# Kernel tuning notes

Measured on AMD Instinct MI355X. Metric: run time of the kernel, lower is better.

The kernel has to match this reference:

```python
import jax, jax.numpy as jnp
import numpy as np

B, S, D, F, E = 2, 1024, 1024, 4096, 8

def setup_inputs() -> dict:
    key = jax.random.key(0)
    ks = jax.random.split(key, 6)
    sc = 0.02  # typical init scale
    return {
        "sequences": jax.random.normal(ks[0], (B, S, D), jnp.float32),
        "router_w1": jax.random.normal(ks[1], (D, D), jnp.float32) * sc,
        "router_b1": jnp.zeros((D,), jnp.float32),
        "router_w2": jax.random.normal(ks[2], (D, E), jnp.float32) * sc,
        "router_b2": jnp.zeros((E,), jnp.float32),
        "expert_w1": jax.random.normal(ks[3], (E, D, F), jnp.float32) * sc,
        "expert_b1": jnp.zeros((E, F), jnp.float32),
        "expert_w2": jax.random.normal(ks[4], (E, F, D), jnp.float32) * sc,
        "expert_b2": jnp.zeros((E, D), jnp.float32),
    }

def reference(sequences, router_w1, router_b1, router_w2, router_b2,
              expert_w1, expert_b1, expert_w2, expert_b2):
    # Router: Linear -> ReLU -> Linear -> Softmax, per-token argmax expert pick
    h = jax.nn.relu(sequences @ router_w1 + router_b1)          # [B,S,D]
    probs = jax.nn.softmax(h @ router_w2 + router_b2, axis=-1)  # [B,S,E]
    idx = jnp.argmax(probs, axis=-1)                            # [B,S] int
    onehot = jax.nn.one_hot(idx, expert_w1.shape[0], dtype=sequences.dtype)  # [B,S,E]
    # Dense all-expert FFN (2-layer position-wise FC w/ ReLU, dropout=0 eval),
    # then combine with the one-hot selection (hard top-1 dispatch semantics).
    hid = jax.nn.relu(jnp.einsum('bsd,edf->ebsf', sequences, expert_w1)
                      + expert_b1[:, None, None, :])            # [E,B,S,F]
    y = jnp.einsum('ebsf,efd->ebsd', hid, expert_w2) + expert_b2[:, None, None, :]
    return jnp.einsum('ebsd,bse->bsd', y, onehot)               # [B,S,D]
```

## Files before the change

kernel.cpp:

```cpp
#include <hip/hip_runtime.h>
#include <hip/hip_bf16.h>

#define T_TOK 2048
#define DD 1024
#define FF 4096
#define EE 8

typedef __attribute__((ext_vector_type(8))) short short8;
typedef __attribute__((ext_vector_type(4))) short short4v;
typedef __attribute__((ext_vector_type(4))) float floatx4;

static __device__ __forceinline__ unsigned f2bf_u(float f){
  unsigned u = __float_as_uint(f);
  unsigned r = u + 0x7fffu + ((u >> 16) & 1u);
  return r >> 16;
}

static __device__ __forceinline__ short8 ldfrag(const unsigned short* p){
  short4v lo = *(const short4v*)p;
  short4v hi = *(const short4v*)(p + 4);
  return __builtin_shufflevector(lo, hi, 0, 1, 2, 3, 4, 5, 6, 7);
}

__global__ __launch_bounds__(256) void router_gemm1(
    const float* __restrict__ X, const float* __restrict__ W,
    const float* __restrict__ bias, float* __restrict__ H, int* counts)
{
  if (blockIdx.x == 0 && blockIdx.y == 0 && threadIdx.x < EE) counts[threadIdx.x] = 0;
  __shared__ float As[2][16][68];
  __shared__ float Bs[2][16][68];
  const int tid = threadIdx.x;
  const int tx = tid & 15, ty = tid >> 4;
  const int bm = blockIdx.y * 64, bn = blockIdx.x * 64;
  const int ar = tid >> 2, ak = (tid & 3) * 4;
  const int bk = tid >> 4, bn0 = (tid & 15) * 4;
  const float* aP = X + (size_t)(bm + ar) * DD;
  float acc[4][4] = {};
  float4 pa, pb;

  pa = *(const float4*)(aP + ak);
  pb = *(const float4*)(W + (size_t)bk * DD + bn + bn0);
  As[0][ak+0][ar] = pa.x; As[0][ak+1][ar] = pa.y;
  As[0][ak+2][ar] = pa.z; As[0][ak+3][ar] = pa.w;
  *(float4*)&Bs[0][bk][bn0] = pb;
  __syncthreads();

  for (int it = 0; it < DD/16; ++it){
    if (it + 1 < DD/16){
      const int kt = (it + 1) * 16;
      pa = *(const float4*)(aP + kt + ak);
      pb = *(const float4*)(W + (size_t)(kt + bk) * DD + bn + bn0);
    }
    const int buf = it & 1;
    #pragma unroll
    for (int k = 0; k < 16; ++k){
      float4 av = *(const float4*)&As[buf][k][ty*4];
      float4 bv = *(const float4*)&Bs[buf][k][tx*4];
      float am[4] = {av.x, av.y, av.z, av.w};
      float bm4[4] = {bv.x, bv.y, bv.z, bv.w};
      #pragma unroll
      for (int i = 0; i < 4; ++i)
        #pragma unroll
        for (int j = 0; j < 4; ++j)
          acc[i][j] += am[i] * bm4[j];
    }
    if (it + 1 < DD/16){
      const int nb2 = (it + 1) & 1;
      As[nb2][ak+0][ar] = pa.x; As[nb2][ak+1][ar] = pa.y;
      As[nb2][ak+2][ar] = pa.z; As[nb2][ak+3][ar] = pa.w;
      *(float4*)&Bs[nb2][bk][bn0] = pb;
      __syncthreads();
    }
  }
  #pragma unroll
  for (int i = 0; i < 4; ++i){
    float4 v;
    v.x = fmaxf(acc[i][0] + bias[bn + tx*4 + 0], 0.f);
    v.y = fmaxf(acc[i][1] + bias[bn + tx*4 + 1], 0.f);
    v.z = fmaxf(acc[i][2] + bias[bn + tx*4 + 2], 0.f);
    v.w = fmaxf(acc[i][3] + bias[bn + tx*4 + 3], 0.f);
    *(float4*)(H + (size_t)(bm + ty*4 + i) * DD + bn + tx*4) = v;
  }
}

__global__ __launch_bounds__(64) void router_logits_argmax(
    const float* __restrict__ H, const float* __restrict__ W2,
    const float* __restrict__ b2, int* __restrict__ eidx, int* __restrict__ counts)
{
  const int t = blockIdx.x;
  const int lane = threadIdx.x;
  const float* h = H + (size_t)t * DD;
  float acc[8] = {0,0,0,0,0,0,0,0};
  for (int d = lane; d < DD; d += 64){
    float hv = h[d];
    float4 w0 = *(const float4*)(W2 + (size_t)d * 8);
    float4 w1 = *(const float4*)(W2 + (size_t)d * 8 + 4);
    acc[0] += hv * w0.x; acc[1] += hv * w0.y; acc[2] += hv * w0.z; acc[3] += hv * w0.w;
    acc[4] += hv * w1.x; acc[5] += hv * w1.y; acc[6] += hv * w1.z; acc[7] += hv * w1.w;
  }
  #pragma unroll
  for (int s = 32; s > 0; s >>= 1)
    #pragma unroll
    for (int e2 = 0; e2 < 8; ++e2)
      acc[e2] += __shfl_down(acc[e2], s, 64);
  if (lane == 0){
    int best = 0; float bv = acc[0] + b2[0];
    #pragma unroll
    for (int e2 = 1; e2 < 8; ++e2){
      float v = acc[e2] + b2[e2];
      if (v > bv){ bv = v; best = e2; }
    }
    eidx[t] = best;
    atomicAdd(&counts[best], 1);
  }
}

__global__ void scan_offsets(const int* __restrict__ counts, int* __restrict__ offsets,
                             int* __restrict__ cursors)
{
  if (threadIdx.x == 0 && blockIdx.x == 0){
    int s = 0;
    for (int e = 0; e < EE; ++e){ offsets[e] = s; cursors[e] = s; s += counts[e]; }
    offsets[EE] = s;
  }
}

__global__ __launch_bounds__(256) void scatter_tokens(
    const int* __restrict__ eidx, int* __restrict__ cursors, int* __restrict__ perm)
{
  int t = blockIdx.x * 256 + threadIdx.x;
  if (t < T_TOK){
    int e = eidx[t];
    int p = atomicAdd(&cursors[e], 1);
    perm[p] = t;
  }
}

template<bool FIRST>
__global__ __launch_bounds__(256) void expert_gemm(
    const float* __restrict__ X,
    const unsigned short* __restrict__ hidIn,
    const float* __restrict__ Wall,
    const float* __restrict__ Ball,
    unsigned short* __restrict__ hidOut,
    float* __restrict__ Yout,
    const int* __restrict__ perm,
    const int* __restrict__ offsets)
{
  constexpr int K = FIRST ? DD : FF;
  constexpr int N = FIRST ? FF : DD;
  constexpr int NIT = K / 64;
  const int e   = blockIdx.z;
  const int off = offsets[e];
  const int cnt = offsets[e+1] - off;
  const int m0  = blockIdx.y * 64;
  if (m0 >= cnt) return;
  const int nb = blockIdx.x * 64;
  const float* W    = Wall + (size_t)e * K * N;
  const float* bias = Ball + (size_t)e * N;

  __shared__ unsigned short As[2][64 * 68];
  __shared__ unsigned short Bs[2][64 * 68];

  const int tid = threadIdx.x;
  const int ar = tid >> 2;
  const int ak = (tid & 3) * 16;
  int mrow = m0 + ar; if (mrow >= cnt) mrow = cnt - 1;
  const float* aF = nullptr;
  const unsigned short* aH = nullptr;
  if constexpr (FIRST) aF = X + (size_t)perm[off + mrow] * DD;
  else                 aH = hidIn + (size_t)(off + mrow) * FF;
  const int bkp = (tid >> 3) * 2;
  const int bn0 = (tid & 7) * 8;

  const int lane = tid & 63;
  const int w    = tid >> 6;
  const int wm   = (w & 1) * 32;
  const int wn   = (w >> 1) * 32;
  const int lrow = lane & 15;
  const int lq   = lane >> 4;

  floatx4 acc[2][2];
  #pragma unroll
  for (int i = 0; i < 2; ++i)
    #pragma unroll
    for (int j = 0; j < 2; ++j)
      acc[i][j] = (floatx4){0.f, 0.f, 0.f, 0.f};

  float4 fa[4]; uint4 ha[2];
  float4 fb[4];

  auto issue = [&](int kt){
    if constexpr (FIRST){
      #pragma unroll
      for (int i = 0; i < 4; ++i) fa[i] = *(const float4*)(aF + kt + ak + i*4);
    } else {
      ha[0] = *(const uint4*)(aH + kt + ak);
      ha[1] = *(const uint4*)(aH + kt + ak + 8);
    }
    const float* r0 = W + (size_t)(kt + bkp) * N + nb + bn0;
    fb[0] = *(const float4*)(r0);
    fb[1] = *(const float4*)(r0 + 4);
    fb[2] = *(const float4*)(r0 + N);
    fb[3] = *(const float4*)(r0 + N + 4);
  };

  auto stage = [&](int buf){
    unsigned short* a = &As[buf][ar*68 + ak];
    if constexpr (FIRST){
      #pragma unroll
      for (int i = 0; i < 4; ++i){
        const float* f = (const float*)&fa[i];
        uint2 p;
        p.x = f2bf_u(f[0]) | (f2bf_u(f[1]) << 16);
        p.y = f2bf_u(f[2]) | (f2bf_u(f[3]) << 16);
        *(uint2*)(a + i*4) = p;
      }
    } else {
      *(uint2*)(a + 0)  = make_uint2(ha[0].x, ha[0].y);
      *(uint2*)(a + 4)  = make_uint2(ha[0].z, ha[0].w);
      *(uint2*)(a + 8)  = make_uint2(ha[1].x, ha[1].y);
      *(uint2*)(a + 12) = make_uint2(ha[1].z, ha[1].w);
    }
    const float* l0 = (const float*)&fb[0];
    const float* l1 = (const float*)&fb[1];
    const float* h0 = (const float*)&fb[2];
    const float* h1 = (const float*)&fb[3];
    #pragma unroll
    for (int j = 0; j < 4; ++j){
      *(unsigned*)(&Bs[buf][(bn0 + j)*68 + bkp])     = f2bf_u(l0[j]) | (f2bf_u(h0[j]) << 16);
      *(unsigned*)(&Bs[buf][(bn0 + 4 + j)*68 + bkp]) = f2bf_u(l1[j]) | (f2bf_u(h1[j]) << 16);
    }
  };

  auto compute = [&](int buf){
    #pragma unroll
    for (int ks = 0; ks < 2; ++ks){
      short8 afr[2], bfr[2];
      #pragma unroll
      for (int i = 0; i < 2; ++i)
        afr[i] = ldfrag(&As[buf][(wm + i*16 + lrow)*68 + ks*32 + lq*8]);
      #pragma unroll
      for (int j = 0; j < 2; ++j)
        bfr[j] = ldfrag(&Bs[buf][(wn + j*16 + lrow)*68 + ks*32 + lq*8]);
      #pragma unroll
      for (int i = 0; i < 2; ++i)
        #pragma unroll
        for (int j = 0; j < 2; ++j)
          acc[i][j] = __builtin_amdgcn_mfma_f32_16x16x32_bf16(afr[i], bfr[j], acc[i][j], 0, 0, 0);
    }
  };

  issue(0);
  stage(0);
  __syncthreads();
  for (int it = 0; it < NIT; ++it){
    if (it + 1 < NIT) issue((it + 1) * 64);
    compute(it & 1);
    if (it + 1 < NIT){
      stage((it + 1) & 1);
      __syncthreads();
    }
  }

  #pragma unroll
  for (int i = 0; i < 2; ++i){
    #pragma unroll
    for (int j = 0; j < 2; ++j){
      const int n = nb + wn + j*16 + lrow;
      const float bv = bias[n];
      #pragma unroll
      for (int r = 0; r < 4; ++r){
        int m = m0 + wm + i*16 + lq*4 + r;
        if (m < cnt){
          float v = acc[i][j][r] + bv;
          if constexpr (FIRST){
            v = fmaxf(v, 0.f);
            hidOut[(size_t)(off + m) * FF + n] = (unsigned short)f2bf_u(v);
          } else {
            Yout[(size_t)perm[off + m] * DD + n] = v;
          }
        }
      }
    }
  }
}

extern "C" void kernel_launch(void* const* d_in, const int* in_sizes, int n_in,
                              void* d_out, int out_size, void* d_ws, size_t ws_size,
                              hipStream_t stream)
{
  const float* X   = (const float*)d_in[0];
  const float* rw1 = (const float*)d_in[1];
  const float* rb1 = (const float*)d_in[2];
  const float* rw2 = (const float*)d_in[3];
  const float* rb2 = (const float*)d_in[4];
  const float* ew1 = (const float*)d_in[5];
  const float* eb1 = (const float*)d_in[6];
  const float* ew2 = (const float*)d_in[7];
  const float* eb2 = (const float*)d_in[8];
  float* out = (float*)d_out;

  char* w = (char*)d_ws;
  float* H = (float*)w;                       w += (size_t)T_TOK * DD * sizeof(float);
  unsigned short* hid = (unsigned short*)w;   w += (size_t)T_TOK * FF * sizeof(short);
  int* eidx    = (int*)w;  w += T_TOK * sizeof(int);
  int* perm    = (int*)w;  w += T_TOK * sizeof(int);
  int* counts  = (int*)w;  w += 16 * sizeof(int);
  int* offsets = (int*)w;  w += 16 * sizeof(int);
  int* cursors = (int*)w;

  router_gemm1<<<dim3(DD/64, T_TOK/64), 256, 0, stream>>>(X, rw1, rb1, H, counts);
  router_logits_argmax<<<dim3(T_TOK), 64, 0, stream>>>(H, rw2, rb2, eidx, counts);
  scan_offsets<<<1, 64, 0, stream>>>(counts, offsets, cursors);
  scatter_tokens<<<dim3(T_TOK/256), 256, 0, stream>>>(eidx, cursors, perm);
  expert_gemm<true ><<<dim3(FF/64, T_TOK/64, EE), 256, 0, stream>>>(X, nullptr, ew1, eb1, hid, nullptr, perm, offsets);
  expert_gemm<false><<<dim3(DD/64, T_TOK/64, EE), 256, 0, stream>>>(nullptr, hid, ew2, eb2, nullptr, out, perm, offsets);
}
```

Measured before the change: 514.6 us.

## Rework MoE pipeline with compact expert slots, split-K, async LDS loads

Replaces the router GEMM with a 128x128 split-K version whose partial sums are reduced, with bias and ReLU applied, inside the logits kernel. Tokens are gathered and converted to bf16 once up front. The expert GEMMs now use 128-row tiles over a compact list of (expert, m0) slots instead of a dense E x M grid, and load A through global_load_lds into a swizzled LDS layout. The second expert GEMM optionally splits K in two and adds a separate reduction kernel. The aim is to cut wasted blocks, redundant fp32-to-bf16 conversion and low occupancy, at the cost of extra partial-sum traffic and more kernel launches.

```diff
diff --git a/kernel.cpp b/kernel.cpp
--- a/kernel.cpp
+++ b/kernel.cpp
@@ -1,25 +1,34 @@
 #include <hip/hip_runtime.h>
-#include <hip/hip_bf16.h>
 
 #define T_TOK 2048
 #define DD 1024
 #define FF 4096
 #define EE 8
+#define MT 128
+#define MAX_SLOTS 24
 
 typedef __attribute__((ext_vector_type(8))) short short8;
 typedef __attribute__((ext_vector_type(4))) short short4v;
 typedef __attribute__((ext_vector_type(4))) float floatx4;
-
-static __device__ __forceinline__ unsigned f2bf_u(float f){
-  unsigned u = __float_as_uint(f);
-  unsigned r = u + 0x7fffu + ((u >> 16) & 1u);
+typedef unsigned int u32;
+typedef unsigned short u16;
+
+static __device__ __forceinline__ u32 f2bf_u(float f){
+  u32 u = __float_as_uint(f);
+  u32 r = u + 0x7fffu + ((u >> 16) & 1u);
   return r >> 16;
 }
 
-static __device__ __forceinline__ short8 ldfrag(const unsigned short* p){
+static __device__ __forceinline__ short8 ldfrag(const u16* p){
   short4v lo = *(const short4v*)p;
   short4v hi = *(const short4v*)(p + 4);
   return __builtin_shufflevector(lo, hi, 0, 1, 2, 3, 4, 5, 6, 7);
+}
+
+static __device__ __forceinline__ void async_copy16(const void* g, void* l){
+  __builtin_amdgcn_global_load_lds(
+      (const __attribute__((address_space(1))) u32*)g,
+      (__attribute__((address_space(3))) u32*)l, 16, 0, 0);
 }
 
 __global__ __launch_bounds__(256) void router_gemm1(
@@ -83,16 +92,91 @@
   }
 }
 
+__global__ __launch_bounds__(256) void router_gemm1_sk(
+    const float* __restrict__ X, const float* __restrict__ W,
+    float* __restrict__ Hp, int* counts)
+{
+  if (blockIdx.x == 0 && blockIdx.y == 0 && blockIdx.z == 0 && threadIdx.x < EE)
+    counts[threadIdx.x] = 0;
+  __shared__ float As[2][16][132];
+  __shared__ float Bs[2][16][132];
+  const int tid = threadIdx.x;
+  const int tx = tid & 15, ty = tid >> 4;
+  const int bm = blockIdx.y * 128, bn = blockIdx.x * 128;
+  const int kbase = blockIdx.z * (DD/4);
+  const int ar = tid >> 2, ak = (tid & 3) * 4;
+  const int bk = tid >> 4, bn0 = (tid & 15) * 8;
+  float acc[8][8] = {};
+  float4 pa0, pa1, pb0, pb1;
+
+  auto issue = [&](int kt){
+    pa0 = *(const float4*)(X + (size_t)(bm + ar)      * DD + kbase + kt + ak);
+    pa1 = *(const float4*)(X + (size_t)(bm + ar + 64) * DD + kbase + kt + ak);
+    const float* wp = W + (size_t)(kbase + kt + bk) * DD + bn + bn0;
+    pb0 = *(const float4*)wp;
+    pb1 = *(const float4*)(wp + 4);
+  };
+  auto stage = [&](int buf){
+    float a0[4] = {pa0.x, pa0.y, pa0.z, pa0.w};
+    float a1[4] = {pa1.x, pa1.y, pa1.z, pa1.w};
+    #pragma unroll
+    for (int j = 0; j < 4; ++j){
+      As[buf][ak+j][ar]      = a0[j];
+      As[buf][ak+j][ar + 64] = a1[j];
+    }
+    *(float4*)&Bs[buf][bk][bn0]     = pb0;
+    *(float4*)&Bs[buf][bk][bn0 + 4] = pb1;
+  };
+
+  issue(0); stage(0); __syncthreads();
+  const int NIT = (DD/4)/16;
+  for (int it = 0; it < NIT; ++it){
+    if (it + 1 < NIT) issue((it + 1) * 16);
+    const int buf = it & 1;
+    #pragma unroll
+    for (int k = 0; k < 16; ++k){
+      float4 av0 = *(const float4*)&As[buf][k][ty*8];
+      float4 av1 = *(const float4*)&As[buf][k][ty*8 + 4];
+      float4 bv0 = *(const float4*)&Bs[buf][k][tx*8];
+      float4 bv1 = *(const float4*)&Bs[buf][k][tx*8 + 4];
+      float a[8] = {av0.x, av0.y, av0.z, av0.w, av1.x, av1.y, av1.z, av1.w};
+      float b[8] = {bv0.x, bv0.y, bv0.z, bv0.w, bv1.x, bv1.y, bv1.z, bv1.w};
+      #pragma unroll
+      for (int i = 0; i < 8; ++i)
+        #pragma unroll
+        for (int j = 0; j < 8; ++j)
+          acc[i][j] += a[i] * b[j];
+    }
+    if (it + 1 < NIT){ stage((it + 1) & 1); __syncthreads(); }
+  }
+  float* o = Hp + (size_t)blockIdx.z * T_TOK * DD;
+  #pragma unroll
+  for (int i = 0; i < 8; ++i){
+    float4 v0 = {acc[i][0], acc[i][1], acc[i][2], acc[i][3]};
+    float4 v1 = {acc[i][4], acc[i][5], acc[i][6], acc[i][7]};
+    *(float4*)(o + (size_t)(bm + ty*8 + i) * DD + bn + tx*8)     = v0;
+    *(float4*)(o + (size_t)(bm + ty*8 + i) * DD + bn + tx*8 + 4) = v1;
+  }
+}
+
+template<bool SK>
 __global__ __launch_bounds__(64) void router_logits_argmax(
-    const float* __restrict__ H, const float* __restrict__ W2,
-    const float* __restrict__ b2, int* __restrict__ eidx, int* __restrict__ counts)
+    const float* __restrict__ Hsrc, const float* __restrict__ b1,
+    const float* __restrict__ W2, const float* __restrict__ b2,
+    int* __restrict__ eidx, int* __restrict__ counts)
 {
   const int t = blockIdx.x;
   const int lane = threadIdx.x;
-  const float* h = H + (size_t)t * DD;
   float acc[8] = {0,0,0,0,0,0,0,0};
   for (int d = lane; d < DD; d += 64){
-    float hv = h[d];
+    float hv;
+    if constexpr (SK){
+      const size_t TD = (size_t)T_TOK * DD;
+      const float* p = Hsrc + (size_t)t * DD + d;
+      hv = fmaxf(p[0] + p[TD] + p[2*TD] + p[3*TD] + b1[d], 0.f);
+    } else {
+      hv = Hsrc[(size_t)t * DD + d];
+    }
     float4 w0 = *(const float4*)(W2 + (size_t)d * 8);
     float4 w1 = *(const float4*)(W2 + (size_t)d * 8 + 4);
     acc[0] += hv * w0.x; acc[1] += hv * w0.y; acc[2] += hv * w0.z; acc[3] += hv * w0.w;
@@ -116,12 +200,18 @@
 }
 
 __global__ void scan_offsets(const int* __restrict__ counts, int* __restrict__ offsets,
-                             int* __restrict__ cursors)
+                             int* __restrict__ cursors, int* __restrict__ slot_e,
+                             int* __restrict__ slot_m0, int* __restrict__ nslots)
 {
   if (threadIdx.x == 0 && blockIdx.x == 0){
-    int s = 0;
-    for (int e = 0; e < EE; ++e){ offsets[e] = s; cursors[e] = s; s += counts[e]; }
+    int s = 0, ns = 0;
+    for (int e = 0; e < EE; ++e){
+      offsets[e] = s; cursors[e] = s;
+      for (int m0 = 0; m0 < counts[e]; m0 += MT){ slot_e[ns] = e; slot_m0[ns] = m0; ++ns; }
+      s += counts[e];
+    }
     offsets[EE] = s;
+    *nslots = ns;
   }
 }
 
@@ -136,154 +226,194 @@
   }
 }
 
+__global__ __launch_bounds__(256) void gather_convert_x(
+    const float* __restrict__ X, const int* __restrict__ perm, u16* __restrict__ Xp)
+{
+  const int p = blockIdx.x;
+  const int t = perm[p];
+  const float4 v = *(const float4*)(X + (size_t)t * DD + threadIdx.x * 4);
+  u32 w0 = f2bf_u(v.x) | (f2bf_u(v.y) << 16);
+  u32 w1 = f2bf_u(v.z) | (f2bf_u(v.w) << 16);
+  *(uint2*)(Xp + (size_t)p * DD + threadIdx.x * 4) = make_uint2(w0, w1);
+}
+
 template<bool FIRST>
 __global__ __launch_bounds__(256) void expert_gemm(
-    const float* __restrict__ X,
-    const unsigned short* __restrict__ hidIn,
+    const u16*  __restrict__ Ap,
     const float* __restrict__ Wall,
     const float* __restrict__ Ball,
-    unsigned short* __restrict__ hidOut,
+    u16*  __restrict__ hidOut,
     float* __restrict__ Yout,
+    float* __restrict__ Part,
     const int* __restrict__ perm,
-    const int* __restrict__ offsets)
-{
-  constexpr int K = FIRST ? DD : FF;
-  constexpr int N = FIRST ? FF : DD;
-  constexpr int NIT = K / 64;
-  const int e   = blockIdx.z;
+    const int* __restrict__ offsets,
+    const int* __restrict__ slot_e,
+    const int* __restrict__ slot_m0,
+    const int* __restrict__ nslots,
+    const int gridK)
+{
+  constexpr int K  = FIRST ? DD : FF;
+  constexpr int N  = FIRST ? FF : DD;
+  constexpr int NW = FIRST ? 128 : 64;
+  constexpr int NJ = NW / 32;
+
+  const int slot = blockIdx.y;
+  if (slot >= *nslots) return;
+  const int e   = slot_e[slot];
+  const int m0  = slot_m0[slot];
   const int off = offsets[e];
   const int cnt = offsets[e+1] - off;
-  const int m0  = blockIdx.y * 64;
-  if (m0 >= cnt) return;
-  const int nb = blockIdx.x * 64;
-  const float* W    = Wall + (size_t)e * K * N;
-  const float* bias = Ball + (size_t)e * N;
-
-  __shared__ unsigned short As[2][64 * 68];
-  __shared__ unsigned short Bs[2][64 * 68];
-
-  const int tid = threadIdx.x;
-  const int ar = tid >> 2;
-  const int ak = (tid & 3) * 16;
-  int mrow = m0 + ar; if (mrow >= cnt) mrow = cnt - 1;
-  const float* aF = nullptr;
-  const unsigned short* aH = nullptr;
-  if constexpr (FIRST) aF = X + (size_t)perm[off + mrow] * DD;
-  else                 aH = hidIn + (size_t)(off + mrow) * FF;
-  const int bkp = (tid >> 3) * 2;
-  const int bn0 = (tid & 7) * 8;
-
+  const int nb  = blockIdx.x * NW;
+  const int kc  = blockIdx.z;
+  const int Kc  = FIRST ? K : (K / gridK);
+  const int kb  = kc * Kc;
+  const int NIT = Kc / 32;
+  const float* W = Wall + (size_t)e * K * N;
+
+  __shared__ u16 As[2][MT * 32];
+  __shared__ u16 Bs[2][NW * 36];
+
+  const int tid  = threadIdx.x;
   const int lane = tid & 63;
-  const int w    = tid >> 6;
-  const int wm   = (w & 1) * 32;
-  const int wn   = (w >> 1) * 32;
+  const int wv   = tid >> 6;
+
+  const u16* asrc[2];
+  #pragma unroll
+  for (int s = 0; s < 2; ++s){
+    const int wi = wv * 2 + s;
+    const int r  = wi * 16 + (lane >> 2);
+    const int q  = (lane & 3) ^ ((r >> 1) & 3);
+    int rowg = off + m0 + r;
+    if (rowg > T_TOK - 1) rowg = T_TOK - 1;
+    asrc[s] = Ap + (size_t)rowg * K + kb + q * 8;
+  }
+  auto stageA = [&](int buf, int it){
+    #pragma unroll
+    for (int s = 0; s < 2; ++s)
+      async_copy16(asrc[s] + it * 32, &As[buf][(wv * 2 + s) * 512]);
+  };
+
+  const int dk2 = tid >> 4;
+  const int bn0 = (tid & 15) * (NW / 16);
+  float4 fb0, fb1, fb2, fb3;
+  auto issueB = [&](int it){
+    const float* r0 = W + (size_t)(kb + it * 32 + 2 * dk2) * N + nb + bn0;
+    fb0 = *(const float4*)r0;
+    fb2 = *(const float4*)(r0 + N);
+    if constexpr (FIRST){
+      fb1 = *(const float4*)(r0 + 4);
+      fb3 = *(const float4*)(r0 + N + 4);
+    }
+  };
+  auto stageB = [&](int buf){
+    float l0[4] = {fb0.x, fb0.y, fb0.z, fb0.w};
+    float h0[4] = {fb2.x, fb2.y, fb2.z, fb2.w};
+    #pragma unroll
+    for (int j = 0; j < 4; ++j)
+      *(u32*)&Bs[buf][(bn0 + j) * 36 + 2 * dk2] = f2bf_u(l0[j]) | (f2bf_u(h0[j]) << 16);
+    if constexpr (FIRST){
+      float l1[4] = {fb1.x, fb1.y, fb1.z, fb1.w};
+      float h1[4] = {fb3.x, fb3.y, fb3.z, fb3.w};
+      #pragma unroll
+      for (int j = 0; j < 4; ++j)
+        *(u32*)&Bs[buf][(bn0 + 4 + j) * 36 + 2 * dk2] = f2bf_u(l1[j]) | (f2bf_u(h1[j]) << 16);
+    }
+  };
+
+  const int wm   = (wv & 1) * 64;
+  const int wn   = (wv >> 1) * (FIRST ? 64 : 32);
   const int lrow = lane & 15;
   const int lq   = lane >> 4;
 
-  floatx4 acc[2][2];
-  #pragma unroll
-  for (int i = 0; i < 2; ++i)
-    #pragma unroll
-    for (int j = 0; j < 2; ++j)
+  floatx4 acc[4][NJ];
+  #pragma unroll
+  for (int i = 0; i < 4; ++i)
+    #pragma unroll
+    for (int j = 0; j < NJ; ++j)
       acc[i][j] = (floatx4){0.f, 0.f, 0.f, 0.f};
 
-  float4 fa[4]; uint4 ha[2];
-  float4 fb[4];
-
-  auto issue = [&](int kt){
-    if constexpr (FIRST){
+  auto compute = [&](int buf){
+    short8 af[4], bfr[NJ];
+    #pragma unroll
+    for (int i = 0; i < 4; ++i){
+      const int r  = wm + i * 16 + lrow;
+      const int sl = lq ^ ((r >> 1) & 3);
+      af[i] = *(const short8*)&As[buf][r * 32 + sl * 8];
+    }
+    #pragma unroll
+    for (int j = 0; j < NJ; ++j){
+      const int nn = wn + j * 16 + lrow;
+      bfr[j] = ldfrag(&Bs[buf][nn * 36 + lq * 8]);
+    }
+    #pragma unroll
+    for (int i = 0; i < 4; ++i)
       #pragma unroll
-      for (int i = 0; i < 4; ++i) fa[i] = *(const float4*)(aF + kt + ak + i*4);
-    } else {
-      ha[0] = *(const uint4*)(aH + kt + ak);
-      ha[1] = *(const uint4*)(aH + kt + ak + 8);
-    }
-    const float* r0 = W + (size_t)(kt + bkp) * N + nb + bn0;
-    fb[0] = *(const float4*)(r0);
-    fb[1] = *(const float4*)(r0 + 4);
-    fb[2] = *(const float4*)(r0 + N);
-    fb[3] = *(const float4*)(r0 + N + 4);
-  };
-
-  auto stage = [&](int buf){
-    unsigned short* a = &As[buf][ar*68 + ak];
-    if constexpr (FIRST){
-      #pragma unroll
-      for (int i = 0; i < 4; ++i){
-        const float* f = (const float*)&fa[i];
-        uint2 p;
-        p.x = f2bf_u(f[0]) | (f2bf_u(f[1]) << 16);
-        p.y = f2bf_u(f[2]) | (f2bf_u(f[3]) << 16);
-        *(uint2*)(a + i*4) = p;
-      }
-    } else {
-      *(uint2*)(a + 0)  = make_uint2(ha[0].x, ha[0].y);
-      *(uint2*)(a + 4)  = make_uint2(ha[0].z, ha[0].w);
-      *(uint2*)(a + 8)  = make_uint2(ha[1].x, ha[1].y);
-      *(uint2*)(a + 12) = make_uint2(ha[1].z, ha[1].w);
-    }
-    const float* l0 = (const float*)&fb[0];
-    const float* l1 = (const float*)&fb[1];
-    const float* h0 = (const float*)&fb[2];
-    const float* h1 = (const float*)&fb[3];
-    #pragma unroll
-    for (int j = 0; j < 4; ++j){
-      *(unsigned*)(&Bs[buf][(bn0 + j)*68 + bkp])     = f2bf_u(l0[j]) | (f2bf_u(h0[j]) << 16);
-      *(unsigned*)(&Bs[buf][(bn0 + 4 + j)*68 + bkp]) = f2bf_u(l1[j]) | (f2bf_u(h1[j]) << 16);
-    }
-  };
-
-  auto compute = [&](int buf){
-    #pragma unroll
-    for (int ks = 0; ks < 2; ++ks){
-      short8 afr[2], bfr[2];
-      #pragma unroll
-      for (int i = 0; i < 2; ++i)
-        afr[i] = ldfrag(&As[buf][(wm + i*16 + lrow)*68 + ks*32 + lq*8]);
-      #pragma unroll
-      for (int j = 0; j < 2; ++j)
-        bfr[j] = ldfrag(&Bs[buf][(wn + j*16 + lrow)*68 + ks*32 + lq*8]);
-      #pragma unroll
-      for (int i = 0; i < 2; ++i)
-        #pragma unroll
-        for (int j = 0; j < 2; ++j)
-          acc[i][j] = __builtin_amdgcn_mfma_f32_16x16x32_bf16(afr[i], bfr[j], acc[i][j], 0, 0, 0);
-    }
-  };
-
-  issue(0);
-  stage(0);
+      for (int j = 0; j < NJ; ++j)
+        acc[i][j] = __builtin_amdgcn_mfma_f32_16x16x32_bf16(af[i], bfr[j], acc[i][j], 0, 0, 0);
+  };
+
+  issueB(0);
+  stageA(0, 0);
+  stageB(0);
   __syncthreads();
   for (int it = 0; it < NIT; ++it){
-    if (it + 1 < NIT) issue((it + 1) * 64);
-    compute(it & 1);
+    const int buf = it & 1;
     if (it + 1 < NIT){
-      stage((it + 1) & 1);
+      issueB(it + 1);
+      stageA(buf ^ 1, it + 1);
+    }
+    compute(buf);
+    if (it + 1 < NIT){
+      stageB(buf ^ 1);
       __syncthreads();
     }
   }
 
   #pragma unroll
-  for (int i = 0; i < 2; ++i){
-    #pragma unroll
-    for (int j = 0; j < 2; ++j){
-      const int n = nb + wn + j*16 + lrow;
-      const float bv = bias[n];
+  for (int i = 0; i < 4; ++i){
+    #pragma unroll
+    for (int j = 0; j < NJ; ++j){
+      const int n = nb + wn + j * 16 + lrow;
+      const float bv = Ball[(size_t)e * N + n];
       #pragma unroll
       for (int r = 0; r < 4; ++r){
-        int m = m0 + wm + i*16 + lq*4 + r;
+        const int m = m0 + wm + i * 16 + lq * 4 + r;
         if (m < cnt){
-          float v = acc[i][j][r] + bv;
+          float v = acc[i][j][r];
           if constexpr (FIRST){
-            v = fmaxf(v, 0.f);
-            hidOut[(size_t)(off + m) * FF + n] = (unsigned short)f2bf_u(v);
+            v = fmaxf(v + bv, 0.f);
+            hidOut[(size_t)(off + m) * FF + n] = (u16)f2bf_u(v);
           } else {
-            Yout[(size_t)perm[off + m] * DD + n] = v;
+            if (gridK == 1){
+              Yout[(size_t)perm[off + m] * DD + n] = v + bv;
+            } else {
+              Part[(size_t)kc * T_TOK * DD + (size_t)(off + m) * DD + n] = v;
+            }
           }
         }
       }
     }
   }
+}
+
+__global__ __launch_bounds__(256) void reduce_second(
+    const float* __restrict__ Part, const float* __restrict__ Ball,
+    const int* __restrict__ perm, const int* __restrict__ eidx,
+    float* __restrict__ out)
+{
+  const int p = blockIdx.x;
+  const int t = perm[p];
+  const int e = eidx[t];
+  const int d = threadIdx.x * 4;
+  const float4 v0 = *(const float4*)(Part + (size_t)p * DD + d);
+  const float4 v1 = *(const float4*)(Part + (size_t)T_TOK * DD + (size_t)p * DD + d);
+  const float4 bb = *(const float4*)(Ball + (size_t)e * DD + d);
+  float4 o;
+  o.x = v0.x + v1.x + bb.x;
+  o.y = v0.y + v1.y + bb.y;
+  o.z = v0.z + v1.z + bb.z;
+  o.w = v0.w + v1.w + bb.w;
+  *(float4*)(out + (size_t)t * DD + d) = o;
 }
 
 extern "C" void kernel_launch(void* const* d_in, const int* in_sizes, int n_in,
@@ -301,19 +431,51 @@
   const float* eb2 = (const float*)d_in[8];
   float* out = (float*)d_out;
 
+  const size_t MB = (size_t)1 << 20;
+  const bool fast = ws_size >= 48 * MB + 65536;
+
   char* w = (char*)d_ws;
-  float* H = (float*)w;                       w += (size_t)T_TOK * DD * sizeof(float);
-  unsigned short* hid = (unsigned short*)w;   w += (size_t)T_TOK * FF * sizeof(short);
-  int* eidx    = (int*)w;  w += T_TOK * sizeof(int);
-  int* perm    = (int*)w;  w += T_TOK * sizeof(int);
-  int* counts  = (int*)w;  w += 16 * sizeof(int);
-  int* offsets = (int*)w;  w += 16 * sizeof(int);
-  int* cursors = (int*)w;
-
-  router_gemm1<<<dim3(DD/64, T_TOK/64), 256, 0, stream>>>(X, rw1, rb1, H, counts);
-  router_logits_argmax<<<dim3(T_TOK), 64, 0, stream>>>(H, rw2, rb2, eidx, counts);
-  scan_offsets<<<1, 64, 0, stream>>>(counts, offsets, cursors);
+  float* rpart = nullptr; float* H = nullptr; float* epart = nullptr;
+  u16* Xp; u16* hid; char* intbase;
+  if (fast){
+    rpart = (float*)w;
+    Xp    = (u16*)w;
+    epart = (float*)(w + 4 * MB);
+    hid   = (u16*)(w + 32 * MB);
+    intbase = w + 48 * MB;
+  } else {
+    H   = (float*)w;
+    Xp  = (u16*)w;
+    hid = (u16*)(w + 8 * MB);
+    intbase = w + 24 * MB;
+  }
+  int* ip      = (int*)intbase;
+  int* eidx    = ip;  ip += T_TOK;
+  int* perm    = ip;  ip += T_TOK;
+  int* counts  = ip;  ip += 16;
+  int* offsets = ip;  ip += 16;
+  int* cursors = ip;  ip += 16;
+  int* slot_e  = ip;  ip += 32;
+  int* slot_m0 = ip;  ip += 32;
+  int* nslots  = ip;  ip += 4;
+
+  if (fast){
+    router_gemm1_sk<<<dim3(DD/128, T_TOK/128, 4), 256, 0, stream>>>(X, rw1, rpart, counts);
+    router_logits_argmax<true><<<dim3(T_TOK), 64, 0, stream>>>(rpart, rb1, rw2, rb2, eidx, counts);
+  } else {
+    router_gemm1<<<dim3(DD/64, T_TOK/64), 256, 0, stream>>>(X, rw1, rb1, H, counts);
+    router_logits_argmax<false><<<dim3(T_TOK), 64, 0, stream>>>(H, rb1, rw2, rb2, eidx, counts);
+  }
+  scan_offsets<<<dim3(1), 64, 0, stream>>>(counts, offsets, cursors, slot_e, slot_m0, nslots);
   scatter_tokens<<<dim3(T_TOK/256), 256, 0, stream>>>(eidx, cursors, perm);
-  expert_gemm<true ><<<dim3(FF/64, T_TOK/64, EE), 256, 0, stream>>>(X, nullptr, ew1, eb1, hid, nullptr, perm, offsets);
-  expert_gemm<false><<<dim3(DD/64, T_TOK/64, EE), 256, 0, stream>>>(nullptr, hid, ew2, eb2, nullptr, out, perm, offsets);
-}
+  gather_convert_x<<<dim3(T_TOK), 256, 0, stream>>>(X, perm, Xp);
+
+  expert_gemm<true><<<dim3(FF/128, MAX_SLOTS, 1), 256, 0, stream>>>(
+      Xp, ew1, eb1, hid, nullptr, nullptr, perm, offsets, slot_e, slot_m0, nslots, 1);
+
+  const int gk = fast ? 2 : 1;
+  expert_gemm<false><<<dim3(DD/64, MAX_SLOTS, gk), 256, 0, stream>>>(
+      hid, ew2, eb2, nullptr, out, epart, perm, offsets, slot_e, slot_m0, nslots, gk);
+  if (fast)
+    reduce_second<<<dim3(T_TOK), 256, 0, stream>>>(epart, eb2, perm, eidx, out);
+}
```

Result: no change. 512.2 us (-0.5%).
